# Optimization experiments

Measured on AMD Instinct MI355X. Metric: run time of the kernel, lower is better.

Reference implementation:

```python
import jax, jax.numpy as jnp
import numpy as np

N_NODES = 100000


def _add_self_loops(edge_index, n):
    loops = jnp.arange(n, dtype=edge_index.dtype)
    row = jnp.concatenate([edge_index[0], loops])
    col = jnp.concatenate([edge_index[1], loops])
    return row, col


def _gcn_norm(row, col, n):
    # symmetric normalization deg^-1/2 on A + I (PyG GCNConv default)
    deg = jax.ops.segment_sum(jnp.ones_like(col, dtype=jnp.float32), col, num_segments=n)
    dinv = jnp.where(deg > 0, jax.lax.rsqrt(deg), 0.0)
    return dinv[row] * dinv[col]  # [E']


def _gcn_conv(x, W, b, row, col, norm, n):
    xw = x @ W                                   # [N, out]
    msg = norm[:, None] * xw[row]                # gather + edge scale, [E', out]
    agg = jax.ops.segment_sum(msg, col, num_segments=n)  # scatter-add, [N, out]
    return agg + b


def setup_inputs() -> dict:
    key = jax.random.key(0)
    ks = jax.random.split(key, 10)
    n, e, f, c = N_NODES, 6400000, 128, 4
    x = jax.random.normal(ks[0], (n, f), dtype=jnp.float32)
    edge_index = jax.random.randint(ks[1], (2, e), 0, n, dtype=jnp.int64)
    def glorot(k, shp):
        lim = float(np.sqrt(6.0 / (shp[0] + shp[1])))
        return jax.random.uniform(k, shp, jnp.float32, -lim, lim)
    return {
        "x": x, "edge_index": edge_index,
        "W1": glorot(ks[2], (f, 4)), "b1": jnp.zeros((4,), jnp.float32),
        "W2": glorot(ks[3], (4, 4)), "b2": jnp.zeros((4,), jnp.float32),
        "W3": glorot(ks[4], (4, 2)), "b3": jnp.zeros((2,), jnp.float32),
        "Wc": glorot(ks[5], (2, c)), "bc": jnp.zeros((c,), jnp.float32),
    }


def reference(x, edge_index, W1, b1, W2, b2, W3, b3, Wc, bc):
    n = x.shape[0]
    row, col = _add_self_loops(edge_index, n)
    norm = _gcn_norm(row, col, n)
    y1 = jax.nn.relu(_gcn_conv(x, W1, b1, row, col, norm, n))
    y2 = jax.nn.relu(_gcn_conv(y1, W2, b2, row, col, norm, n))
    y3 = jax.nn.relu(_gcn_conv(y2, W3, b3, row, col, norm, n))
    out = y3 @ Wc + bc
    return out, y3
```

## Files before the change

### kernel.cpp

```cpp
#include <hip/hip_runtime.h>
#include <stdint.h>

#define TPB 256
#define SPAN 256
#define LSH 8
#define PART_B 256
#define PART_T 1024
#define SCAN_T 1024
#define SCAN_B 4096
#define SORT_CAP 18432



__global__ __launch_bounds__(PART_T) void p_hist(
    const int* __restrict__ col, uint32_t* __restrict__ H,
    int NB, int E, int PBE) {
    __shared__ uint32_t cnt[1024];
    for (int i = threadIdx.x; i < NB; i += PART_T) cnt[i] = 0u;
    __syncthreads();
    int blk = blockIdx.x;
    int s = blk * PBE, e = min(E, s + PBE);
    for (int i = s + threadIdx.x; i < e; i += PART_T)
        atomicAdd(&cnt[col[i] >> LSH], 1u);
    __syncthreads();
    for (int i = threadIdx.x; i < NB; i += PART_T)
        H[(size_t)i * PART_B + blk] = cnt[i];
}

__global__ __launch_bounds__(SCAN_T) void k_scan1(
    const unsigned int* __restrict__ in, unsigned int* __restrict__ partial,
    unsigned int* __restrict__ bsum, int M) {
    __shared__ unsigned int sm[SCAN_T];
    int tid  = threadIdx.x;
    int base = blockIdx.x * SCAN_B + tid * 4;
    unsigned int v0 = (base + 0 < M) ? in[base + 0] : 0u;
    unsigned int v1 = (base + 1 < M) ? in[base + 1] : 0u;
    unsigned int v2 = (base + 2 < M) ? in[base + 2] : 0u;
    unsigned int v3 = (base + 3 < M) ? in[base + 3] : 0u;
    unsigned int s = v0 + v1 + v2 + v3;
    sm[tid] = s;
    __syncthreads();
    for (int off = 1; off < SCAN_T; off <<= 1) {
        unsigned int t = (tid >= off) ? sm[tid - off] : 0u;
        __syncthreads();
        sm[tid] += t;
        __syncthreads();
    }
    unsigned int excl = sm[tid] - s;
    if (base + 0 < M) partial[base + 0] = excl;
    if (base + 1 < M) partial[base + 1] = excl + v0;
    if (base + 2 < M) partial[base + 2] = excl + v0 + v1;
    if (base + 3 < M) partial[base + 3] = excl + v0 + v1 + v2;
    if (tid == SCAN_T - 1) bsum[blockIdx.x] = sm[SCAN_T - 1];
}

__global__ void k_scan2(unsigned int* __restrict__ bsum, int nb) {
    if (threadIdx.x == 0 && blockIdx.x == 0) {
        unsigned int run = 0;
        for (int i = 0; i < nb; ++i) {
            unsigned int t = bsum[i];
            bsum[i] = run;
            run += t;
        }
    }
}

__global__ __launch_bounds__(TPB) void k_scan3(
    const unsigned int* __restrict__ partial, const unsigned int* __restrict__ bsum,
    unsigned int* __restrict__ outp, int M, int E) {
    int i = blockIdx.x * TPB + threadIdx.x;
    if (i < M) outp[i] = partial[i] + bsum[i / SCAN_B];
    if (i == 0) outp[M] = (unsigned int)E;
}

__global__ __launch_bounds__(PART_T) void p_part(
    const int* __restrict__ row, const int* __restrict__ col,
    const uint32_t* __restrict__ O, uint32_t* __restrict__ bpack,
    int NB, int E, int PBE) {
    __shared__ uint32_t cur[1024];
    int blk = blockIdx.x;
    for (int i = threadIdx.x; i < NB; i += PART_T)
        cur[i] = O[(size_t)i * PART_B + blk];
    __syncthreads();
    int s = blk * PBE, e = min(E, s + PBE);
    for (int i = s + threadIdx.x; i < e; i += PART_T) {
        int c = col[i];
        uint32_t slot = atomicAdd(&cur[c >> LSH], 1u);
        bpack[slot] = ((uint32_t)row[i] << LSH) | (uint32_t)(c & (SPAN - 1));
    }
}

extern __shared__ uint32_t sort_buf[];
__global__ __launch_bounds__(PART_T) void p_sort(
    const uint32_t* __restrict__ bpack, const uint32_t* __restrict__ O,
    int* __restrict__ csr_row, unsigned int* __restrict__ indptr,
    float* __restrict__ dinv, int NB, int N, int E) {
    __shared__ uint32_t hist[SPAN];
    __shared__ uint32_t cur[SPAN];
    int b = blockIdx.x;
    int t = threadIdx.x;
    if (t < SPAN) hist[t] = 0u;
    __syncthreads();
    uint32_t s = O[(size_t)b * PART_B];
    uint32_t e = (b + 1 < NB) ? O[(size_t)(b + 1) * PART_B] : (uint32_t)E;
    uint32_t W = e - s;
    for (uint32_t i = s + t; i < e; i += PART_T)
        atomicAdd(&hist[bpack[i] & (SPAN - 1)], 1u);
    __syncthreads();
    if (t < SPAN) cur[t] = hist[t];
    __syncthreads();
    for (int off = 1; off < SPAN; off <<= 1) {
        uint32_t v = (t < SPAN && t >= off) ? cur[t - off] : 0u;
        __syncthreads();
        if (t < SPAN) cur[t] += v;
        __syncthreads();
    }
    if (t < SPAN) {
        uint32_t excl = cur[t] - hist[t];
        int n = b * SPAN + t;
        if (n < N) {
            indptr[n] = s + excl;
            dinv[n]   = rsqrtf((float)(hist[t] + 1u));
            if (n == N - 1) indptr[N] = (unsigned int)E;
        }
        cur[t] = excl;
    }
    __syncthreads();
    if (W <= SORT_CAP) {
        for (uint32_t i = s + t; i < e; i += PART_T) {
            uint32_t v = bpack[i];
            uint32_t slot = atomicAdd(&cur[v & (SPAN - 1)], 1u);
            sort_buf[slot] = v >> LSH;
        }
        __syncthreads();
        for (uint32_t j = t; j < W; j += PART_T)
            csr_row[s + j] = (int)sort_buf[j];
    } else {
        for (uint32_t i = s + t; i < e; i += PART_T) {
            uint32_t v = bpack[i];
            uint32_t slot = atomicAdd(&cur[v & (SPAN - 1)], 1u);
            csr_row[s + slot] = (int)(v >> LSH);
        }
    }
}


__global__ __launch_bounds__(TPB) void k_xw1d(
    const float* __restrict__ x, const float* __restrict__ W1,
    const float* __restrict__ dinv, float* __restrict__ dxw1, int N) {
    __shared__ float sW[512];
    for (int t = threadIdx.x; t < 512; t += TPB) sW[t] = W1[t];
    __syncthreads();
    int gid  = blockIdx.x * TPB + threadIdx.x;
    int node = gid >> 6;
    int lane = threadIdx.x & 63;
    if (node >= N) return;
    float2 v = *(const float2*)(x + (size_t)node * 128 + 2 * lane);
    const float* w0 = &sW[(2 * lane) * 4];
    const float* w1 = &sW[(2 * lane + 1) * 4];
    float a[4];
#pragma unroll
    for (int j = 0; j < 4; ++j) a[j] = v.x * w0[j] + v.y * w1[j];
#pragma unroll
    for (int off = 32; off > 0; off >>= 1) {
#pragma unroll
        for (int j = 0; j < 4; ++j) a[j] += __shfl_down(a[j], off);
    }
    if (lane == 0) {
        float d = dinv[node];
        *(float4*)(dxw1 + (size_t)node * 4) =
            make_float4(d * a[0], d * a[1], d * a[2], d * a[3]);
    }
}

__global__ __launch_bounds__(TPB) void k_gather44(
    const unsigned int* __restrict__ indptr, const int* __restrict__ csr_row,
    const float* __restrict__ dinv, const float* __restrict__ dxw_in,
    const float* __restrict__ b, const float* __restrict__ W,
    float* __restrict__ dxw_out, int N) {
    int gid  = blockIdx.x * TPB + threadIdx.x;
    int node = gid >> 4;
    int sub  = gid & 15;
    if (node >= N) return;
    int e0 = (int)indptr[node], e1 = (int)indptr[node + 1];
    float4 acc = make_float4(0.f, 0.f, 0.f, 0.f);
    for (int j = e0 + sub; j < e1; j += 16) {
        int r = csr_row[j];
        float4 m = *(const float4*)(dxw_in + (size_t)r * 4);
        acc.x += m.x; acc.y += m.y; acc.z += m.z; acc.w += m.w;
    }
#pragma unroll
    for (int off = 1; off < 16; off <<= 1) {
        acc.x += __shfl_xor(acc.x, off);
        acc.y += __shfl_xor(acc.y, off);
        acc.z += __shfl_xor(acc.z, off);
        acc.w += __shfl_xor(acc.w, off);
    }
    if (sub == 0) {
        float d = dinv[node];
        float4 sv = *(const float4*)(dxw_in + (size_t)node * 4);
        float h0 = fmaxf(d * (acc.x + sv.x) + b[0], 0.f);
        float h1 = fmaxf(d * (acc.y + sv.y) + b[1], 0.f);
        float h2 = fmaxf(d * (acc.z + sv.z) + b[2], 0.f);
        float h3 = fmaxf(d * (acc.w + sv.w) + b[3], 0.f);
        float o[4];
#pragma unroll
        for (int j = 0; j < 4; ++j)
            o[j] = h0 * W[0 * 4 + j] + h1 * W[1 * 4 + j] +
                   h2 * W[2 * 4 + j] + h3 * W[3 * 4 + j];
        *(float4*)(dxw_out + (size_t)node * 4) =
            make_float4(d * o[0], d * o[1], d * o[2], d * o[3]);
    }
}

__global__ __launch_bounds__(TPB) void k_gather42(
    const unsigned int* __restrict__ indptr, const int* __restrict__ csr_row,
    const float* __restrict__ dinv, const float* __restrict__ dxw_in,
    const float* __restrict__ b, const float* __restrict__ W,
    float* __restrict__ dxw_out, int N) {
    int gid  = blockIdx.x * TPB + threadIdx.x;
    int node = gid >> 4;
    int sub  = gid & 15;
    if (node >= N) return;
    int e0 = (int)indptr[node], e1 = (int)indptr[node + 1];
    float4 acc = make_float4(0.f, 0.f, 0.f, 0.f);
    for (int j = e0 + sub; j < e1; j += 16) {
        int r = csr_row[j];
        float4 m = *(const float4*)(dxw_in + (size_t)r * 4);
        acc.x += m.x; acc.y += m.y; acc.z += m.z; acc.w += m.w;
    }
#pragma unroll
    for (int off = 1; off < 16; off <<= 1) {
        acc.x += __shfl_xor(acc.x, off);
        acc.y += __shfl_xor(acc.y, off);
        acc.z += __shfl_xor(acc.z, off);
        acc.w += __shfl_xor(acc.w, off);
    }
    if (sub == 0) {
        float d = dinv[node];
        float4 sv = *(const float4*)(dxw_in + (size_t)node * 4);
        float h0 = fmaxf(d * (acc.x + sv.x) + b[0], 0.f);
        float h1 = fmaxf(d * (acc.y + sv.y) + b[1], 0.f);
        float h2 = fmaxf(d * (acc.z + sv.z) + b[2], 0.f);
        float h3 = fmaxf(d * (acc.w + sv.w) + b[3], 0.f);
        float o0 = h0 * W[0] + h1 * W[2] + h2 * W[4] + h3 * W[6];
        float o1 = h0 * W[1] + h1 * W[3] + h2 * W[5] + h3 * W[7];
        *(float2*)(dxw_out + (size_t)node * 2) = make_float2(d * o0, d * o1);
    }
}

__global__ __launch_bounds__(TPB) void k_gather2out(
    const unsigned int* __restrict__ indptr, const int* __restrict__ csr_row,
    const float* __restrict__ dinv, const float* __restrict__ dxw3,
    const float* __restrict__ b3, const float* __restrict__ Wc,
    const float* __restrict__ bc,
    float* __restrict__ out, float* __restrict__ y3out, int N) {
    int gid  = blockIdx.x * TPB + threadIdx.x;
    int node = gid >> 4;
    int sub  = gid & 15;
    if (node >= N) return;
    int e0 = (int)indptr[node], e1 = (int)indptr[node + 1];
    float ax = 0.f, ay = 0.f;
    for (int j = e0 + sub; j < e1; j += 16) {
        int r = csr_row[j];
        float2 m = *(const float2*)(dxw3 + (size_t)r * 2);
        ax += m.x; ay += m.y;
    }
#pragma unroll
    for (int off = 1; off < 16; off <<= 1) {
        ax += __shfl_xor(ax, off);
        ay += __shfl_xor(ay, off);
    }
    if (sub == 0) {
        float d = dinv[node];
        float2 sv = *(const float2*)(dxw3 + (size_t)node * 2);
        float y0 = fmaxf(d * (ax + sv.x) + b3[0], 0.f);
        float y1 = fmaxf(d * (ay + sv.y) + b3[1], 0.f);
        float o[4];
#pragma unroll
        for (int j = 0; j < 4; ++j)
            o[j] = y0 * Wc[0 * 4 + j] + y1 * Wc[1 * 4 + j] + bc[j];
        *(float4*)(out + (size_t)node * 4) = make_float4(o[0], o[1], o[2], o[3]);
        *(float2*)(y3out + (size_t)node * 2) = make_float2(y0, y1);
    }
}


__global__ __launch_bounds__(TPB) void k_zero_deg(unsigned int* __restrict__ deg, int N) {
    int i = blockIdx.x * TPB + threadIdx.x;
    if (i < N) deg[i] = 0u;
}

__global__ __launch_bounds__(TPB) void k_deg(
    const int* __restrict__ col, unsigned int* __restrict__ deg, int E) {
    int e = blockIdx.x * TPB + threadIdx.x;
    if (e >= E) return;
    atomicAdd(&deg[col[e]], 1u);
}

__global__ __launch_bounds__(TPB) void k_dinv(const unsigned int* __restrict__ deg,
                                              float* __restrict__ dinv, int N) {
    int i = blockIdx.x * TPB + threadIdx.x;
    if (i < N) dinv[i] = rsqrtf((float)(deg[i] + 1u));
}

__global__ __launch_bounds__(TPB) void k_xw1(
    const float* __restrict__ x, const float* __restrict__ W1,
    const float* __restrict__ dinv,
    float* __restrict__ xw, float* __restrict__ agg, int N) {
    __shared__ float sW[512];
    for (int t = threadIdx.x; t < 512; t += TPB) sW[t] = W1[t];
    __syncthreads();
    int gid  = blockIdx.x * TPB + threadIdx.x;
    int node = gid >> 6;
    int lane = threadIdx.x & 63;
    if (node >= N) return;
    float2 v = *(const float2*)(x + (size_t)node * 128 + 2 * lane);
    const float* w0 = &sW[(2 * lane) * 4];
    const float* w1 = &sW[(2 * lane + 1) * 4];
    float a[4];
#pragma unroll
    for (int j = 0; j < 4; ++j) a[j] = v.x * w0[j] + v.y * w1[j];
#pragma unroll
    for (int off = 32; off > 0; off >>= 1) {
#pragma unroll
        for (int j = 0; j < 4; ++j) a[j] += __shfl_down(a[j], off);
    }
    if (lane == 0) {
        float d  = dinv[node];
        float d2 = d * d;
        *(float4*)(xw  + (size_t)node * 4) = make_float4(a[0], a[1], a[2], a[3]);
        *(float4*)(agg + (size_t)node * 4) =
            make_float4(d2 * a[0], d2 * a[1], d2 * a[2], d2 * a[3]);
    }
}

__global__ __launch_bounds__(TPB) void k_prop4(
    const int* __restrict__ row, const int* __restrict__ col,
    const float* __restrict__ dinv,
    const float* __restrict__ xw, float* __restrict__ agg, int E) {
    int e = blockIdx.x * TPB + threadIdx.x;
    if (e >= E) return;
    int r = row[e];
    int c = col[e];
    float nv = dinv[r] * dinv[c];
    float4 m = *(const float4*)(xw + (size_t)r * 4);
    float* a = agg + (size_t)c * 4;
    atomicAdd(a + 0, nv * m.x);
    atomicAdd(a + 1, nv * m.y);
    atomicAdd(a + 2, nv * m.z);
    atomicAdd(a + 3, nv * m.w);
}

__global__ __launch_bounds__(TPB) void k_prop2(
    const int* __restrict__ row, const int* __restrict__ col,
    const float* __restrict__ dinv,
    const float* __restrict__ xw2, float* __restrict__ agg2, int E) {
    int e = blockIdx.x * TPB + threadIdx.x;
    if (e >= E) return;
    int r = row[e];
    int c = col[e];
    float nv = dinv[r] * dinv[c];
    float2 m = *(const float2*)(xw2 + (size_t)r * 2);
    float* a = agg2 + (size_t)c * 2;
    atomicAdd(a + 0, nv * m.x);
    atomicAdd(a + 1, nv * m.y);
}

__global__ __launch_bounds__(TPB) void k_node2(
    const float* __restrict__ b1, const float* __restrict__ W2,
    const float* __restrict__ dinv,
    float* __restrict__ xw, float* __restrict__ agg, int N) {
    int i = blockIdx.x * TPB + threadIdx.x;
    if (i >= N) return;
    float4 av = *(const float4*)(agg + (size_t)i * 4);
    float h0 = fmaxf(av.x + b1[0], 0.f);
    float h1 = fmaxf(av.y + b1[1], 0.f);
    float h2 = fmaxf(av.z + b1[2], 0.f);
    float h3 = fmaxf(av.w + b1[3], 0.f);
    float o[4];
#pragma unroll
    for (int j = 0; j < 4; ++j)
        o[j] = h0 * W2[0 * 4 + j] + h1 * W2[1 * 4 + j] +
               h2 * W2[2 * 4 + j] + h3 * W2[3 * 4 + j];
    float d  = dinv[i];
    float d2 = d * d;
    *(float4*)(xw  + (size_t)i * 4) = make_float4(o[0], o[1], o[2], o[3]);
    *(float4*)(agg + (size_t)i * 4) = make_float4(d2 * o[0], d2 * o[1], d2 * o[2], d2 * o[3]);
}

__global__ __launch_bounds__(TPB) void k_node3(
    const float* __restrict__ b2, const float* __restrict__ W3,
    const float* __restrict__ dinv,
    const float* __restrict__ agg,
    float* __restrict__ xw3, float* __restrict__ agg3, int N) {
    int i = blockIdx.x * TPB + threadIdx.x;
    if (i >= N) return;
    float4 av = *(const float4*)(agg + (size_t)i * 4);
    float h0 = fmaxf(av.x + b2[0], 0.f);
    float h1 = fmaxf(av.y + b2[1], 0.f);
    float h2 = fmaxf(av.z + b2[2], 0.f);
    float h3 = fmaxf(av.w + b2[3], 0.f);
    float o0 = h0 * W3[0] + h1 * W3[2] + h2 * W3[4] + h3 * W3[6];
    float o1 = h0 * W3[1] + h1 * W3[3] + h2 * W3[5] + h3 * W3[7];
    float d  = dinv[i];
    float d2 = d * d;
    *(float2*)(xw3  + (size_t)i * 2) = make_float2(o0, o1);
    *(float2*)(agg3 + (size_t)i * 2) = make_float2(d2 * o0, d2 * o1);
}

__global__ __launch_bounds__(TPB) void k_out(
    const float* __restrict__ b3, const float* __restrict__ Wc,
    const float* __restrict__ bc,
    const float* __restrict__ agg3,
    float* __restrict__ out, float* __restrict__ y3out, int N) {
    int i = blockIdx.x * TPB + threadIdx.x;
    if (i >= N) return;
    float2 av = *(const float2*)(agg3 + (size_t)i * 2);
    float y0 = fmaxf(av.x + b3[0], 0.f);
    float y1 = fmaxf(av.y + b3[1], 0.f);
    float o[4];
#pragma unroll
    for (int j = 0; j < 4; ++j)
        o[j] = y0 * Wc[0 * 4 + j] + y1 * Wc[1 * 4 + j] + bc[j];
    *(float4*)(out + (size_t)i * 4) = make_float4(o[0], o[1], o[2], o[3]);
    *(float2*)(y3out + (size_t)i * 2) = make_float2(y0, y1);
}

extern "C" void kernel_launch(void* const* d_in, const int* in_sizes, int n_in,
                              void* d_out, int out_size, void* d_ws, size_t ws_size,
                              hipStream_t stream) {
    const float* x  = (const float*)d_in[0];
    const int*   ei = (const int*)d_in[1];
    const float* W1 = (const float*)d_in[2];
    const float* b1 = (const float*)d_in[3];
    const float* W2 = (const float*)d_in[4];
    const float* b2 = (const float*)d_in[5];
    const float* W3 = (const float*)d_in[6];
    const float* b3 = (const float*)d_in[7];
    const float* Wc = (const float*)d_in[8];
    const float* bc = (const float*)d_in[9];

    const int N = in_sizes[0] / 128;
    const int E = in_sizes[1] / 2;

    const int* row = ei;
    const int* col = ei + (size_t)E;

    const int NB  = (N + SPAN - 1) / SPAN;
    const int M   = NB * PART_B;
    const int PBE = (E + PART_B - 1) / PART_B;

    float* out   = (float*)d_out;
    float* y3out = (float*)d_out + (size_t)N * 4;

    const int nblkN = (N + TPB - 1) / TPB;
    const int nblkE = (E + TPB - 1) / TPB;
    const int nblkW = (N * 64 + TPB - 1) / TPB;
    const int nblkG = (N * 16 + TPB - 1) / TPB;
    const int nblkM = (M + 1 + TPB - 1) / TPB;
    const int nblkS = (M + SCAN_B - 1) / SCAN_B;

    size_t off = 0;
    auto carve = [&](size_t bytes) -> void* {
        void* r = (void*)((char*)d_ws + off);
        off += (bytes + 255) & ~(size_t)255;
        return r;
    };
    float*        dinv    = (float*)carve((size_t)N * 4);
    float*        dxw1    = (float*)carve((size_t)N * 4 * 4);
    float*        dxw2    = (float*)carve((size_t)N * 4 * 4);
    float*        dxw3    = (float*)carve((size_t)N * 2 * 4);
    unsigned int* indptr  = (unsigned int*)carve(((size_t)N + 1) * 4);
    uint32_t*     bsum    = (uint32_t*)carve(256 * 4);
    uint32_t*     Hflat   = (uint32_t*)carve(((size_t)M + 1) * 4);
    uint32_t*     bpack   = (uint32_t*)carve((size_t)E * 4);
    int*          csr_row = (int*)carve((size_t)E * 4);
    bool use_bucket = (off <= ws_size) && (NB <= 1024) && (N < (1 << 23));

    if (use_bucket) {
        size_t sort_lds = (size_t)SORT_CAP * 4;
        hipFuncSetAttribute((const void*)p_sort,
                            hipFuncAttributeMaxDynamicSharedMemorySize,
                            (int)sort_lds);
        p_hist<<<PART_B, PART_T, 0, stream>>>(col, Hflat, NB, E, PBE);
        k_scan1<<<nblkS, SCAN_T, 0, stream>>>(Hflat, Hflat, bsum, M);
        k_scan2<<<1, 32, 0, stream>>>(bsum, nblkS);
        k_scan3<<<nblkM, TPB, 0, stream>>>(Hflat, bsum, Hflat, M, E);
        p_part<<<PART_B, PART_T, 0, stream>>>(row, col, Hflat, bpack, NB, E, PBE);
        p_sort<<<NB, PART_T, sort_lds, stream>>>(bpack, Hflat, csr_row, indptr,
                                                 dinv, NB, N, E);
        k_xw1d<<<nblkW, TPB, 0, stream>>>(x, W1, dinv, dxw1, N);
        k_gather44<<<nblkG, TPB, 0, stream>>>(indptr, csr_row, dinv, dxw1, b1, W2, dxw2, N);
        k_gather42<<<nblkG, TPB, 0, stream>>>(indptr, csr_row, dinv, dxw2, b2, W3, dxw3, N);
        k_gather2out<<<nblkG, TPB, 0, stream>>>(indptr, csr_row, dinv, dxw3, b3, Wc, bc,
                                                out, y3out, N);
    } else {
        size_t foff = 0;
        auto fcarve = [&](size_t bytes) -> void* {
            void* r = (void*)((char*)d_ws + foff);
            foff += (bytes + 255) & ~(size_t)255;
            return r;
        };
        unsigned int* deg   = (unsigned int*)fcarve((size_t)N * 4);
        float*        fdinv = (float*)fcarve((size_t)N * 4);
        float*        xw    = (float*)fcarve((size_t)N * 4 * 4);
        float*        agg   = (float*)fcarve((size_t)N * 4 * 4);
        float*        xw3   = (float*)fcarve((size_t)N * 2 * 4);
        float*        agg3  = (float*)fcarve((size_t)N * 2 * 4);
        k_zero_deg<<<nblkN, TPB, 0, stream>>>(deg, N);
        k_deg<<<nblkE, TPB, 0, stream>>>(col, deg, E);
        k_dinv<<<nblkN, TPB, 0, stream>>>(deg, fdinv, N);
        k_xw1<<<nblkW, TPB, 0, stream>>>(x, W1, fdinv, xw, agg, N);
        k_prop4<<<nblkE, TPB, 0, stream>>>(row, col, fdinv, xw, agg, E);
        k_node2<<<nblkN, TPB, 0, stream>>>(b1, W2, fdinv, xw, agg, N);
        k_prop4<<<nblkE, TPB, 0, stream>>>(row, col, fdinv, xw, agg, E);
        k_node3<<<nblkN, TPB, 0, stream>>>(b2, W3, fdinv, agg, xw3, agg3, N);
        k_prop2<<<nblkE, TPB, 0, stream>>>(row, col, fdinv, xw3, agg3, E);
        k_out<<<nblkN, TPB, 0, stream>>>(b3, Wc, bc, agg3, out, y3out, N);
    }
}
```

Baseline: 208.0 us.

## Fuse histogram into partition with block-local bucket layout, drop global scan chain

Merges the separate column-histogram pass into the partition kernel, which now builds a per-block local histogram and scan and writes bpack in block-local segments instead of globally ordered buckets. A single tiny scan over per-bucket totals replaces the three-kernel global scan. The sort kernel then gathers each bucket's pieces from all 256 partition blocks using per-block offsets. This removes one full read of the column array and several launches, but adds scattered, segmented reads in the sort and global atomics on the bucket totals.

```diff
diff --git a/kernel.cpp b/kernel.cpp
--- a/kernel.cpp
+++ b/kernel.cpp
@@ -6,106 +6,94 @@
 #define LSH 8
 #define PART_B 256
 #define PART_T 1024
-#define SCAN_T 1024
-#define SCAN_B 4096
+#define NBMAX 512
 #define SORT_CAP 18432
 
 
-
-__global__ __launch_bounds__(PART_T) void p_hist(
-    const int* __restrict__ col, uint32_t* __restrict__ H,
-    int NB, int E, int PBE) {
-    __shared__ uint32_t cnt[1024];
-    for (int i = threadIdx.x; i < NB; i += PART_T) cnt[i] = 0u;
-    __syncthreads();
-    int blk = blockIdx.x;
-    int s = blk * PBE, e = min(E, s + PBE);
-    for (int i = s + threadIdx.x; i < e; i += PART_T)
-        atomicAdd(&cnt[col[i] >> LSH], 1u);
-    __syncthreads();
-    for (int i = threadIdx.x; i < NB; i += PART_T)
-        H[(size_t)i * PART_B + blk] = cnt[i];
-}
-
-__global__ __launch_bounds__(SCAN_T) void k_scan1(
-    const unsigned int* __restrict__ in, unsigned int* __restrict__ partial,
-    unsigned int* __restrict__ bsum, int M) {
-    __shared__ unsigned int sm[SCAN_T];
-    int tid  = threadIdx.x;
-    int base = blockIdx.x * SCAN_B + tid * 4;
-    unsigned int v0 = (base + 0 < M) ? in[base + 0] : 0u;
-    unsigned int v1 = (base + 1 < M) ? in[base + 1] : 0u;
-    unsigned int v2 = (base + 2 < M) ? in[base + 2] : 0u;
-    unsigned int v3 = (base + 3 < M) ? in[base + 3] : 0u;
-    unsigned int s = v0 + v1 + v2 + v3;
-    sm[tid] = s;
-    __syncthreads();
-    for (int off = 1; off < SCAN_T; off <<= 1) {
-        unsigned int t = (tid >= off) ? sm[tid - off] : 0u;
-        __syncthreads();
-        sm[tid] += t;
-        __syncthreads();
-    }
-    unsigned int excl = sm[tid] - s;
-    if (base + 0 < M) partial[base + 0] = excl;
-    if (base + 1 < M) partial[base + 1] = excl + v0;
-    if (base + 2 < M) partial[base + 2] = excl + v0 + v1;
-    if (base + 3 < M) partial[base + 3] = excl + v0 + v1 + v2;
-    if (tid == SCAN_T - 1) bsum[blockIdx.x] = sm[SCAN_T - 1];
-}
-
-__global__ void k_scan2(unsigned int* __restrict__ bsum, int nb) {
-    if (threadIdx.x == 0 && blockIdx.x == 0) {
-        unsigned int run = 0;
-        for (int i = 0; i < nb; ++i) {
-            unsigned int t = bsum[i];
-            bsum[i] = run;
-            run += t;
-        }
-    }
-}
-
-__global__ __launch_bounds__(TPB) void k_scan3(
-    const unsigned int* __restrict__ partial, const unsigned int* __restrict__ bsum,
-    unsigned int* __restrict__ outp, int M, int E) {
-    int i = blockIdx.x * TPB + threadIdx.x;
-    if (i < M) outp[i] = partial[i] + bsum[i / SCAN_B];
-    if (i == 0) outp[M] = (unsigned int)E;
+__global__ __launch_bounds__(256) void k_zero32(uint32_t* __restrict__ p, int n) {
+    int i = blockIdx.x * 256 + threadIdx.x;
+    if (i < n) p[i] = 0u;
 }
 
 __global__ __launch_bounds__(PART_T) void p_part(
     const int* __restrict__ row, const int* __restrict__ col,
-    const uint32_t* __restrict__ O, uint32_t* __restrict__ bpack,
-    int NB, int E, int PBE) {
-    __shared__ uint32_t cur[1024];
+    uint32_t* __restrict__ bpack, uint32_t* __restrict__ Pg,
+    uint32_t* __restrict__ Hb, int NB, int E, int PBE) {
+    __shared__ uint32_t hist[NBMAX];
+    __shared__ uint32_t cur[NBMAX];
     int blk = blockIdx.x;
-    for (int i = threadIdx.x; i < NB; i += PART_T)
-        cur[i] = O[(size_t)i * PART_B + blk];
-    __syncthreads();
+    int t   = threadIdx.x;
     int s = blk * PBE, e = min(E, s + PBE);
-    for (int i = s + threadIdx.x; i < e; i += PART_T) {
+    int len = e - s;
+    for (int i = t; i < NB; i += PART_T) hist[i] = 0u;
+    __syncthreads();
+    for (int i = s + t; i < e; i += PART_T)
+        atomicAdd(&hist[col[i] >> LSH], 1u);
+    __syncthreads();
+    if (t < NB) cur[t] = hist[t];
+    __syncthreads();
+    for (int off = 1; off < NB; off <<= 1) {
+        uint32_t v = (t < NB && t >= off) ? cur[t - off] : 0u;
+        __syncthreads();
+        if (t < NB) cur[t] += v;
+        __syncthreads();
+    }
+    if (t < NB) {
+        uint32_t excl = cur[t] - hist[t];
+        Pg[(size_t)blk * (NB + 1) + t] = excl;
+        if (hist[t]) atomicAdd(&Hb[t], hist[t]);
+        cur[t] = (uint32_t)s + excl;
+    }
+    if (t == 0) Pg[(size_t)blk * (NB + 1) + NB] = (uint32_t)len;
+    __syncthreads();
+    for (int i = s + t; i < e; i += PART_T) {
         int c = col[i];
         uint32_t slot = atomicAdd(&cur[c >> LSH], 1u);
         bpack[slot] = ((uint32_t)row[i] << LSH) | (uint32_t)(c & (SPAN - 1));
     }
 }
 
+__global__ __launch_bounds__(NBMAX) void k_scanb(
+    const uint32_t* __restrict__ Hb, uint32_t* __restrict__ Ob, int NB, int E) {
+    __shared__ uint32_t sm[NBMAX];
+    int t = threadIdx.x;
+    uint32_t v = (t < NB) ? Hb[t] : 0u;
+    sm[t] = v;
+    __syncthreads();
+    for (int off = 1; off < NBMAX; off <<= 1) {
+        uint32_t u = (t >= off) ? sm[t - off] : 0u;
+        __syncthreads();
+        sm[t] += u;
+        __syncthreads();
+    }
+    if (t < NB) Ob[t] = sm[t] - v;
+    if (t == 0) Ob[NB] = (uint32_t)E;
+}
+
 extern __shared__ uint32_t sort_buf[];
 __global__ __launch_bounds__(PART_T) void p_sort(
-    const uint32_t* __restrict__ bpack, const uint32_t* __restrict__ O,
+    const uint32_t* __restrict__ bpack, const uint32_t* __restrict__ Pg,
+    const uint32_t* __restrict__ Ob,
     int* __restrict__ csr_row, unsigned int* __restrict__ indptr,
-    float* __restrict__ dinv, int NB, int N, int E) {
+    float* __restrict__ dinv, int NB, int N, int E, int PBE) {
     __shared__ uint32_t hist[SPAN];
     __shared__ uint32_t cur[SPAN];
     int b = blockIdx.x;
     int t = threadIdx.x;
+    int wid  = t >> 6;
+    int lane = t & 63;
     if (t < SPAN) hist[t] = 0u;
     __syncthreads();
-    uint32_t s = O[(size_t)b * PART_B];
-    uint32_t e = (b + 1 < NB) ? O[(size_t)(b + 1) * PART_B] : (uint32_t)E;
-    uint32_t W = e - s;
-    for (uint32_t i = s + t; i < e; i += PART_T)
-        atomicAdd(&hist[bpack[i] & (SPAN - 1)], 1u);
+    uint32_t ub = Ob[b], ue = Ob[b + 1];
+    uint32_t W = ue - ub;
+    for (int blk = wid; blk < PART_B; blk += (PART_T >> 6)) {
+        const uint32_t* pb = Pg + (size_t)blk * (NB + 1);
+        uint32_t o0 = pb[b], o1 = pb[b + 1];
+        uint32_t base = (uint32_t)(blk * PBE) + o0;
+        uint32_t L = o1 - o0;
+        for (uint32_t j = lane; j < L; j += 64)
+            atomicAdd(&hist[bpack[base + j] & (SPAN - 1)], 1u);
+    }
     __syncthreads();
     if (t < SPAN) cur[t] = hist[t];
     __syncthreads();
@@ -119,7 +107,7 @@
         uint32_t excl = cur[t] - hist[t];
         int n = b * SPAN + t;
         if (n < N) {
-            indptr[n] = s + excl;
+            indptr[n] = ub + excl;
             dinv[n]   = rsqrtf((float)(hist[t] + 1u));
             if (n == N - 1) indptr[N] = (unsigned int)E;
         }
@@ -127,19 +115,31 @@
     }
     __syncthreads();
     if (W <= SORT_CAP) {
-        for (uint32_t i = s + t; i < e; i += PART_T) {
-            uint32_t v = bpack[i];
-            uint32_t slot = atomicAdd(&cur[v & (SPAN - 1)], 1u);
-            sort_buf[slot] = v >> LSH;
+        for (int blk = wid; blk < PART_B; blk += (PART_T >> 6)) {
+            const uint32_t* pb = Pg + (size_t)blk * (NB + 1);
+            uint32_t o0 = pb[b], o1 = pb[b + 1];
+            uint32_t base = (uint32_t)(blk * PBE) + o0;
+            uint32_t L = o1 - o0;
+            for (uint32_t j = lane; j < L; j += 64) {
+                uint32_t v = bpack[base + j];
+                uint32_t slot = atomicAdd(&cur[v & (SPAN - 1)], 1u);
+                sort_buf[slot] = v >> LSH;
+            }
         }
         __syncthreads();
         for (uint32_t j = t; j < W; j += PART_T)
-            csr_row[s + j] = (int)sort_buf[j];
+            csr_row[ub + j] = (int)sort_buf[j];
     } else {
-        for (uint32_t i = s + t; i < e; i += PART_T) {
-            uint32_t v = bpack[i];
-            uint32_t slot = atomicAdd(&cur[v & (SPAN - 1)], 1u);
-            csr_row[s + slot] = (int)(v >> LSH);
+        for (int blk = wid; blk < PART_B; blk += (PART_T >> 6)) {
+            const uint32_t* pb = Pg + (size_t)blk * (NB + 1);
+            uint32_t o0 = pb[b], o1 = pb[b + 1];
+            uint32_t base = (uint32_t)(blk * PBE) + o0;
+            uint32_t L = o1 - o0;
+            for (uint32_t j = lane; j < L; j += 64) {
+                uint32_t v = bpack[base + j];
+                uint32_t slot = atomicAdd(&cur[v & (SPAN - 1)], 1u);
+                csr_row[ub + slot] = (int)(v >> LSH);
+            }
         }
     }
 }
@@ -448,18 +448,15 @@
     const int* col = ei + (size_t)E;
 
     const int NB  = (N + SPAN - 1) / SPAN;
-    const int M   = NB * PART_B;
     const int PBE = (E + PART_B - 1) / PART_B;
 
     float* out   = (float*)d_out;
     float* y3out = (float*)d_out + (size_t)N * 4;
 
+    const int nblkW = (N * 64 + TPB - 1) / TPB;
+    const int nblkG = (N * 16 + TPB - 1) / TPB;
     const int nblkN = (N + TPB - 1) / TPB;
     const int nblkE = (E + TPB - 1) / TPB;
-    const int nblkW = (N * 64 + TPB - 1) / TPB;
-    const int nblkG = (N * 16 + TPB - 1) / TPB;
-    const int nblkM = (M + 1 + TPB - 1) / TPB;
-    const int nblkS = (M + SCAN_B - 1) / SCAN_B;
 
     size_t off = 0;
     auto carve = [&](size_t bytes) -> void* {
@@ -472,24 +469,23 @@
     float*        dxw2    = (float*)carve((size_t)N * 4 * 4);
     float*        dxw3    = (float*)carve((size_t)N * 2 * 4);
     unsigned int* indptr  = (unsigned int*)carve(((size_t)N + 1) * 4);
-    uint32_t*     bsum    = (uint32_t*)carve(256 * 4);
-    uint32_t*     Hflat   = (uint32_t*)carve(((size_t)M + 1) * 4);
-    uint32_t*     bpack   = (uint32_t*)carve((size_t)E * 4);
+    uint32_t*     Hb      = (uint32_t*)carve((size_t)(NB + 1) * 4);
+    uint32_t*     Ob      = (uint32_t*)carve((size_t)(NB + 1) * 4);
+    uint32_t*     Pg      = (uint32_t*)carve((size_t)PART_B * (NB + 1) * 4);
+    uint32_t*     bpack   = (uint32_t*)carve((size_t)PART_B * PBE * 4);
     int*          csr_row = (int*)carve((size_t)E * 4);
-    bool use_bucket = (off <= ws_size) && (NB <= 1024) && (N < (1 << 23));
+    bool use_bucket = (off <= ws_size) && (NB <= NBMAX) && (N < (1 << 24));
 
     if (use_bucket) {
         size_t sort_lds = (size_t)SORT_CAP * 4;
         hipFuncSetAttribute((const void*)p_sort,
                             hipFuncAttributeMaxDynamicSharedMemorySize,
                             (int)sort_lds);
-        p_hist<<<PART_B, PART_T, 0, stream>>>(col, Hflat, NB, E, PBE);
-        k_scan1<<<nblkS, SCAN_T, 0, stream>>>(Hflat, Hflat, bsum, M);
-        k_scan2<<<1, 32, 0, stream>>>(bsum, nblkS);
-        k_scan3<<<nblkM, TPB, 0, stream>>>(Hflat, bsum, Hflat, M, E);
-        p_part<<<PART_B, PART_T, 0, stream>>>(row, col, Hflat, bpack, NB, E, PBE);
-        p_sort<<<NB, PART_T, sort_lds, stream>>>(bpack, Hflat, csr_row, indptr,
-                                                 dinv, NB, N, E);
+        k_zero32<<<(NB + 256) / 256, 256, 0, stream>>>(Hb, NB + 1);
+        p_part<<<PART_B, PART_T, 0, stream>>>(row, col, bpack, Pg, Hb, NB, E, PBE);
+        k_scanb<<<1, NBMAX, 0, stream>>>(Hb, Ob, NB, E);
+        p_sort<<<NB, PART_T, sort_lds, stream>>>(bpack, Pg, Ob, csr_row, indptr,
+                                                 dinv, NB, N, E, PBE);
         k_xw1d<<<nblkW, TPB, 0, stream>>>(x, W1, dinv, dxw1, N);
         k_gather44<<<nblkG, TPB, 0, stream>>>(indptr, csr_row, dinv, dxw1, b1, W2, dxw2, N);
         k_gather42<<<nblkG, TPB, 0, stream>>>(indptr, csr_row, dinv, dxw2, b2, W3, dxw3, N);
```

Result: slower. 223.5 us (+7.4%).
